# Kernel optimization log

Measured on AMD Instinct MI355X. Metric: run time of the kernel, lower is better.

Reference implementation:

```python
import jax, jax.numpy as jnp
import numpy as np

EMBED_DIM = 1024
NUM_HEADS = 16
HEAD_DIM = EMBED_DIM // NUM_HEADS  # 64, used only for score scaling
B, S = 4, 2048


def setup_inputs() -> dict:
    key = jax.random.key(0)
    k1, k2, k3, k4 = jax.random.split(key, 4)
    rotation_params = jax.random.normal(k1, (3 * EMBED_DIM * EMBED_DIM,), dtype=jnp.float32) * 0.02
    entangle_params = jax.random.normal(k2, (EMBED_DIM * EMBED_DIM,), dtype=jnp.float32) * 0.02
    inputs = jax.random.normal(k3, (B, S, EMBED_DIM), dtype=jnp.float32)
    gate_w = jax.random.normal(k4, (EMBED_DIM, EMBED_DIM), dtype=jnp.float32) * 0.02
    return {"rotation_params": rotation_params, "entangle_params": entangle_params,
            "inputs": inputs, "gate_w": gate_w}


def reference(rotation_params, entangle_params, inputs, gate_w):
    E = EMBED_DIM
    w_qkv = rotation_params.reshape(3 * E, E)   # nn.Linear weight layout (out, in)
    w_out = entangle_params.reshape(E, E)
    # qkv projection: x @ W^T, then chunk into q, k, v along last dim
    qkv = jnp.einsum('bse,fe->bsf', inputs, w_qkv)  # (B, S, 3E)
    q, k, v = jnp.split(qkv, 3, axis=-1)
    # NOTE: original code does NOT split into heads; attention over full E,
    # scaled by sqrt(head_dim).
    q = q * (1.0 / np.sqrt(HEAD_DIM)).astype(np.float32)
    scores = jnp.einsum('bqe,bke->bqk', q, k)       # (B, S, S)
    attn = jax.nn.softmax(scores, axis=-1)
    attn_out = jnp.einsum('bqk,bke->bqe', attn, v)  # (B, S, E)
    out = jnp.einsum('bse,fe->bsf', attn_out, w_out)
    gate = jax.nn.sigmoid(jnp.einsum('bse,fe->bsf', out, gate_w))
    return gate * out
```

## Files before the change

kernel.cpp:

```cpp
#include <hip/hip_runtime.h>
#include <math.h>

#define EMB 1024
#define NB 4
#define SQ 2048
#define TOK (NB*SQ)

typedef __attribute__((ext_vector_type(8))) short bhalf8;
typedef __attribute__((ext_vector_type(4))) float f32x4;

__device__ __forceinline__ unsigned short f32_to_bf16(float f) {
    unsigned int u = __float_as_uint(f);
    u += 0x7FFFu + ((u >> 16) & 1u);
    return (unsigned short)(u >> 16);
}
__device__ __forceinline__ float bf16_to_f32(unsigned short h) {
    return __uint_as_float(((unsigned int)h) << 16);
}
__device__ __forceinline__ unsigned short f32_to_f16(float f) {
    union { _Float16 h; unsigned short u; } c; c.h = (_Float16)f; return c.u;
}
__device__ __forceinline__ float f16_to_f32(unsigned short u) {
    union { _Float16 h; unsigned short u; } c; c.u = u; return (float)c.h;
}

__global__ __launch_bounds__(256) void convert_all_kernel(
    const float* __restrict__ x,  unsigned short* __restrict__ x_bf,
    const float* __restrict__ rot, const float* __restrict__ ent,
    const float* __restrict__ gw, unsigned short* __restrict__ w_bf) {
    const int EE4 = EMB * EMB / 4;
    const float* src;
    unsigned short* dst;
    float scale = 1.0f;
    int j;
    if (blockIdx.x < TOK*EMB/4/256) {
        src = x; dst = x_bf; j = blockIdx.x * 256 + threadIdx.x;
        float4 v = ((const float4*)src)[j];
        ushort4 o = { f32_to_bf16(v.x), f32_to_bf16(v.y), f32_to_bf16(v.z), f32_to_bf16(v.w) };
        ((ushort4*)dst)[j] = o;
        return;
    }
    const int i = (blockIdx.x - TOK*EMB/4/256) * 256 + threadIdx.x;
    j = i; dst = w_bf;
    if (i < 3 * EE4) {
        src = rot;
        if (i < EE4) scale = 0.125f;
    } else if (i < 4 * EE4) { src = ent; j = i - 3 * EE4; }
    else                    { src = gw;  j = i - 4 * EE4; }
    float4 v = ((const float4*)src)[j];
    ushort4 o;
    o.x = f32_to_bf16(v.x * scale);
    o.y = f32_to_bf16(v.y * scale);
    o.z = f32_to_bf16(v.z * scale);
    o.w = f32_to_bf16(v.w * scale);
    ((ushort4*)dst)[i] = o;
}

__device__ __forceinline__ void async_load16(const unsigned short* gp, unsigned short* lp) {
    __builtin_amdgcn_global_load_lds(
        (const __attribute__((address_space(1))) unsigned int*)gp,
        (__attribute__((address_space(3))) unsigned int*)lp,
        16, 0, 0);
}


#define BAR()  __builtin_amdgcn_s_barrier()
#define LGK0() do { asm volatile("s_waitcnt lgkmcnt(0)" ::: "memory"); \
                    __builtin_amdgcn_sched_barrier(0); } while (0)
#define VMC6() asm volatile("s_waitcnt vmcnt(6)" ::: "memory")
#define VMC0() asm volatile("s_waitcnt vmcnt(0)" ::: "memory")

#define STAGE_A(buf, half, kofs) do { \
    async_load16(aG0 + (half)*aH + (kofs), &As[buf][(half)*8192 +        w*512]); \
    async_load16(aG1 + (half)*aH + (kofs), &As[buf][(half)*8192 + 4096 + w*512]); \
} while (0)
#define STAGE_B(buf, half, kofs) do { \
    async_load16(bG0 + (half)*bH + (kofs), &Bs[buf][(half)*8192 +        w*512]); \
    async_load16(bG1 + (half)*bH + (kofs), &Bs[buf][(half)*8192 + 4096 + w*512]); \
} while (0)

#define READ_A(p) do { \
    af[0][0] = *(const bhalf8*)(aRd + ((p)*2    )*1024 + kqs0); \
    af[0][1] = *(const bhalf8*)(aRd + ((p)*2    )*1024 + kqs1); \
    af[1][0] = *(const bhalf8*)(aRd + ((p)*2 + 1)*1024 + kqs0); \
    af[1][1] = *(const bhalf8*)(aRd + ((p)*2 + 1)*1024 + kqs1); \
} while (0)

#define READ_B() do { \
    _Pragma("unroll") \
    for (int ni_ = 0; ni_ < 4; ++ni_) { \
        bfv[ni_][0] = *(const bhalf8*)(bRd + ni_*1024 + kqs0); \
        bfv[ni_][1] = *(const bhalf8*)(bRd + ni_*1024 + kqs1); \
    } \
} while (0)

#define MFMA16(p) do { \
    __builtin_amdgcn_s_setprio(1); \
    _Pragma("unroll") \
    for (int h_ = 0; h_ < 2; ++h_) { \
        _Pragma("unroll") \
        for (int mi_ = 0; mi_ < 2; ++mi_) { \
            _Pragma("unroll") \
            for (int ni_ = 0; ni_ < 4; ++ni_) \
                acc[(p)*2 + mi_][ni_] = __builtin_amdgcn_mfma_f32_16x16x32_bf16( \
                    af[mi_][h_], bfv[ni_][h_], acc[(p)*2 + mi_][ni_], 0, 0, 0); \
        } \
    } \
    __builtin_amdgcn_s_setprio(0); \
} while (0)

template <int MODE>
__global__ __launch_bounds__(512, 2) void gemm_nt_8p(
    const unsigned short* __restrict__ A,
    const unsigned short* __restrict__ B,
    void* __restrict__ C,
    const unsigned short* __restrict__ Obf,
    float* __restrict__ Fout,
    int M, int N, int K, int lda, int ldb, int ldc,
    long sA, long sB, long sC)
{
    __shared__ __align__(16) unsigned short As[2][16384];
    __shared__ __align__(16) unsigned short Bs[2][16384];

    const int bz = blockIdx.z;
    const unsigned short* Ab = A + (long)bz * sA;
    const unsigned short* Bb = B + (long)bz * sB;
    const int bm = blockIdx.x * 256;
    const int bn = blockIdx.y * 256;
    const int t = threadIdx.x;
    const int w = t >> 6;
    const int l = t & 63;

    const int srow = l >> 3;
    const int scol = (((l & 7) ^ (l >> 3)) * 8);

    const int fr = l & 15;
    const int kqs0 = ((((l >> 4)    ) ^ (l & 7)) * 8);
    const int kqs1 = (((4 + (l >> 4)) ^ (l & 7)) * 8);

    const int wm = (w >> 2) * 128;
    const int wn = (w & 3) * 64;

    f32x4 acc[8][4];
    f32x4 zero = {0.f, 0.f, 0.f, 0.f};
    #pragma unroll
    for (int i = 0; i < 8; ++i)
        #pragma unroll
        for (int j = 0; j < 4; ++j) acc[i][j] = zero;

    const unsigned short* aG0 = Ab + (long)(bm + (    w)*8 + srow) * lda + scol;
    const unsigned short* aG1 = Ab + (long)(bm + (8 + w)*8 + srow) * lda + scol;
    const unsigned short* bG0 = Bb + (long)(bn + (    w)*8 + srow) * ldb + scol;
    const unsigned short* bG1 = Bb + (long)(bn + (8 + w)*8 + srow) * ldb + scol;
    const long aH = (long)128 * lda;
    const long bH = (long)128 * ldb;

    const int nkt = K >> 6;

    STAGE_A(0, 0, 0);  STAGE_A(0, 1, 0);
    STAGE_B(0, 0, 0);  STAGE_B(0, 1, 0);
    STAGE_B(1, 0, 64); STAGE_B(1, 1, 64);
    STAGE_A(1, 0, 64);
    VMC6();
    BAR();

    for (int kt = 0; kt < nkt; ++kt) {
        const int cur = kt & 1, nxt = cur ^ 1;
        const unsigned short* aRd = &As[cur][(wm + fr) * 64];
        const unsigned short* bRd = &Bs[cur][(wn + fr) * 64];
        const bool s1 = (kt + 1 < nkt);
        const bool s2 = (kt + 2 < nkt);
        const int k1 = (kt + 1) << 6;
        const int k2 = (kt + 2) << 6;

        bhalf8 bfv[4][2], af[2][2];

        READ_B();
        READ_A(0);
        if (s1) STAGE_A(nxt, 1, k1);
        BAR(); LGK0();
        MFMA16(0);
        BAR();

        READ_A(1);
        if (s2) STAGE_B(cur, 0, k2);
        BAR(); LGK0();
        MFMA16(1);
        BAR();

        READ_A(2);
        if (s2) STAGE_B(cur, 1, k2);
        BAR(); LGK0();
        MFMA16(2);
        BAR();

        READ_A(3);
        if (s2) { STAGE_A(cur, 0, k2); VMC6(); }
        else    { VMC0(); }
        BAR(); LGK0();
        MFMA16(3);
        BAR();
    }

    const int crow = (l >> 4) * 4;
    const int ccol = l & 15;
    #pragma unroll
    for (int mi = 0; mi < 8; ++mi) {
        #pragma unroll
        for (int ni = 0; ni < 4; ++ni) {
            #pragma unroll
            for (int r = 0; r < 4; ++r) {
                const int gr = bm + wm + mi*16 + crow + r;
                const int gc = bn + wn + ni*16 + ccol;
                const float v = acc[mi][ni][r];
                const long idx = (long)gr * ldc + gc;
                if (MODE == 0) {
                    ((unsigned short*)C)[(long)bz*sC + idx] = f32_to_bf16(v);
                } else if (MODE == 1) {
                    ((unsigned short*)C)[(long)bz*sC + idx] = f32_to_f16(v);
                } else {
                    const float o = bf16_to_f32(Obf[idx]);
                    const float g = 1.0f / (1.0f + __expf(-v));
                    Fout[idx] = g * o;
                }
            }
        }
    }
}

#undef BAR
#undef LGK0
#undef VMC6
#undef VMC0
#undef STAGE_A
#undef STAGE_B
#undef READ_A
#undef READ_B
#undef MFMA16

__global__ __launch_bounds__(256) void softmax_kernel(const unsigned short* __restrict__ sc,
                                                      unsigned short* __restrict__ attn) {
    const long row = blockIdx.x;
    const unsigned short* p = sc + row * SQ;
    unsigned short* q = attn + row * SQ;
    const int t = threadIdx.x;
    const int w = t >> 6, l = t & 63;
    union { bhalf8 v; unsigned short u[8]; } in;
    in.v = ((const bhalf8*)p)[t];
    float f[8];
    float m = -1e30f;
    #pragma unroll
    for (int j = 0; j < 8; ++j) { f[j] = f16_to_f32(in.u[j]); m = fmaxf(m, f[j]); }
    #pragma unroll
    for (int off = 32; off; off >>= 1) m = fmaxf(m, __shfl_xor(m, off));
    __shared__ float smax[4], ssum[4];
    if (l == 0) smax[w] = m;
    __syncthreads();
    m = fmaxf(fmaxf(smax[0], smax[1]), fmaxf(smax[2], smax[3]));
    float s = 0.f;
    #pragma unroll
    for (int j = 0; j < 8; ++j) { f[j] = __expf(f[j] - m); s += f[j]; }
    #pragma unroll
    for (int off = 32; off; off >>= 1) s += __shfl_xor(s, off);
    if (l == 0) ssum[w] = s;
    __syncthreads();
    const float inv = 1.0f / (ssum[0] + ssum[1] + ssum[2] + ssum[3]);
    union { bhalf8 v; unsigned short u[8]; } o;
    #pragma unroll
    for (int j = 0; j < 8; ++j) o.u[j] = f32_to_bf16(f[j] * inv);
    ((bhalf8*)q)[t] = o.v;
}

__global__ void transpose_v(const unsigned short* __restrict__ qkv,
                            unsigned short* __restrict__ vT) {
    __shared__ unsigned short tile[32][33];
    const int b = blockIdx.z;
    const unsigned short* v = qkv + (long)b * SQ * (3*EMB) + 2*EMB;
    const int e = blockIdx.x * 32 + threadIdx.x;
    const int s = blockIdx.y * 32 + threadIdx.y;
    tile[threadIdx.y][threadIdx.x] = v[(long)s * (3*EMB) + e];
    __syncthreads();
    const int so = blockIdx.y * 32 + threadIdx.x;
    const int eo = blockIdx.x * 32 + threadIdx.y;
    vT[(long)b * EMB * SQ + (long)eo * SQ + so] = tile[threadIdx.x][threadIdx.y];
}

extern "C" void kernel_launch(void* const* d_in, const int* in_sizes, int n_in,
                              void* d_out, int out_size, void* d_ws, size_t ws_size,
                              hipStream_t stream) {
    const float* rot = (const float*)d_in[0];
    const float* ent = (const float*)d_in[1];
    const float* x   = (const float*)d_in[2];
    const float* gw  = (const float*)d_in[3];
    float* outp = (float*)d_out;
    char* ws = (char*)d_ws;

    size_t off = 0;
    unsigned short* x_bf    = (unsigned short*)(ws + off); off += (size_t)TOK*EMB*2;
    unsigned short* wqkv_bf = (unsigned short*)(ws + off); off += (size_t)3*EMB*EMB*2;
    unsigned short* wout_bf = (unsigned short*)(ws + off); off += (size_t)EMB*EMB*2;
    unsigned short* gate_bf = (unsigned short*)(ws + off); off += (size_t)EMB*EMB*2;
    unsigned short* qkv_bf  = (unsigned short*)(ws + off); off += (size_t)TOK*3*EMB*2;
    unsigned short* vT_bf   = (unsigned short*)(ws + off); off += (size_t)NB*EMB*SQ*2;
    unsigned short* sc_f16  = (unsigned short*)(ws + off); off += (size_t)NB*SQ*SQ*2;
    unsigned short* attn_bf = qkv_bf;
    unsigned short* ao_bf   = x_bf;
    unsigned short* out_bf  = qkv_bf + (size_t)NB*SQ*SQ;

    convert_all_kernel<<<dim3(TOK*EMB/4/256 + 5*EMB*EMB/4/256), dim3(256), 0, stream>>>(
        x, x_bf, rot, ent, gw, wqkv_bf);

    gemm_nt_8p<0><<<dim3(TOK/256, 3*EMB/256, 1), dim3(512), 0, stream>>>(
        x_bf, wqkv_bf, qkv_bf, nullptr, nullptr,
        TOK, 3*EMB, EMB, EMB, EMB, 3*EMB, 0, 0, 0);

    transpose_v<<<dim3(EMB/32, SQ/32, NB), dim3(32, 32), 0, stream>>>(qkv_bf, vT_bf);

    gemm_nt_8p<1><<<dim3(SQ/256, SQ/256, NB), dim3(512), 0, stream>>>(
        qkv_bf, qkv_bf + EMB, sc_f16, nullptr, nullptr,
        SQ, SQ, EMB, 3*EMB, 3*EMB, SQ,
        (long)SQ*3*EMB, (long)SQ*3*EMB, (long)SQ*SQ);

    softmax_kernel<<<dim3(NB*SQ), dim3(256), 0, stream>>>(sc_f16, attn_bf);

    gemm_nt_8p<0><<<dim3(SQ/256, EMB/256, NB), dim3(512), 0, stream>>>(
        attn_bf, vT_bf, ao_bf, nullptr, nullptr,
        SQ, EMB, SQ, SQ, SQ, EMB,
        (long)SQ*SQ, (long)EMB*SQ, (long)SQ*EMB);

    gemm_nt_8p<0><<<dim3(TOK/256, EMB/256, 1), dim3(512), 0, stream>>>(
        ao_bf, wout_bf, out_bf, nullptr, nullptr,
        TOK, EMB, EMB, EMB, EMB, EMB, 0, 0, 0);

    gemm_nt_8p<2><<<dim3(TOK/256, EMB/256, 1), dim3(512), 0, stream>>>(
        out_bf, gate_bf, nullptr, out_bf, outp,
        TOK, EMB, EMB, EMB, EMB, EMB, 0, 0, 0);
}
```

Measured before the change: 355.0 us.

## Add 128x128 single-buffer GEMM for small-N stages and reschedule 256-tile pipeline

After: 329.6 us. 7.2% less time.

```diff
diff --git a/kernel.cpp b/kernel.cpp
--- a/kernel.cpp
+++ b/kernel.cpp
@@ -63,54 +63,8 @@
         16, 0, 0);
 }
 
-
-#define BAR()  __builtin_amdgcn_s_barrier()
-#define LGK0() do { asm volatile("s_waitcnt lgkmcnt(0)" ::: "memory"); \
-                    __builtin_amdgcn_sched_barrier(0); } while (0)
-#define VMC6() asm volatile("s_waitcnt vmcnt(6)" ::: "memory")
-#define VMC0() asm volatile("s_waitcnt vmcnt(0)" ::: "memory")
-
-#define STAGE_A(buf, half, kofs) do { \
-    async_load16(aG0 + (half)*aH + (kofs), &As[buf][(half)*8192 +        w*512]); \
-    async_load16(aG1 + (half)*aH + (kofs), &As[buf][(half)*8192 + 4096 + w*512]); \
-} while (0)
-#define STAGE_B(buf, half, kofs) do { \
-    async_load16(bG0 + (half)*bH + (kofs), &Bs[buf][(half)*8192 +        w*512]); \
-    async_load16(bG1 + (half)*bH + (kofs), &Bs[buf][(half)*8192 + 4096 + w*512]); \
-} while (0)
-
-#define READ_A(p) do { \
-    af[0][0] = *(const bhalf8*)(aRd + ((p)*2    )*1024 + kqs0); \
-    af[0][1] = *(const bhalf8*)(aRd + ((p)*2    )*1024 + kqs1); \
-    af[1][0] = *(const bhalf8*)(aRd + ((p)*2 + 1)*1024 + kqs0); \
-    af[1][1] = *(const bhalf8*)(aRd + ((p)*2 + 1)*1024 + kqs1); \
-} while (0)
-
-#define READ_B() do { \
-    _Pragma("unroll") \
-    for (int ni_ = 0; ni_ < 4; ++ni_) { \
-        bfv[ni_][0] = *(const bhalf8*)(bRd + ni_*1024 + kqs0); \
-        bfv[ni_][1] = *(const bhalf8*)(bRd + ni_*1024 + kqs1); \
-    } \
-} while (0)
-
-#define MFMA16(p) do { \
-    __builtin_amdgcn_s_setprio(1); \
-    _Pragma("unroll") \
-    for (int h_ = 0; h_ < 2; ++h_) { \
-        _Pragma("unroll") \
-        for (int mi_ = 0; mi_ < 2; ++mi_) { \
-            _Pragma("unroll") \
-            for (int ni_ = 0; ni_ < 4; ++ni_) \
-                acc[(p)*2 + mi_][ni_] = __builtin_amdgcn_mfma_f32_16x16x32_bf16( \
-                    af[mi_][h_], bfv[ni_][h_], acc[(p)*2 + mi_][ni_], 0, 0, 0); \
-        } \
-    } \
-    __builtin_amdgcn_s_setprio(0); \
-} while (0)
-
 template <int MODE>
-__global__ __launch_bounds__(512, 2) void gemm_nt_8p(
+__global__ __launch_bounds__(256) void gemm_nt_128(
     const unsigned short* __restrict__ A,
     const unsigned short* __restrict__ B,
     void* __restrict__ C,
@@ -119,93 +73,68 @@
     int M, int N, int K, int lda, int ldb, int ldc,
     long sA, long sB, long sC)
 {
-    __shared__ __align__(16) unsigned short As[2][16384];
-    __shared__ __align__(16) unsigned short Bs[2][16384];
+    __shared__ __align__(16) unsigned short As[128*64];
+    __shared__ __align__(16) unsigned short Bs[128*64];
 
     const int bz = blockIdx.z;
     const unsigned short* Ab = A + (long)bz * sA;
     const unsigned short* Bb = B + (long)bz * sB;
-    const int bm = blockIdx.x * 256;
-    const int bn = blockIdx.y * 256;
+    const int bm = blockIdx.x * 128;
+    const int bn = blockIdx.y * 128;
     const int t = threadIdx.x;
     const int w = t >> 6;
     const int l = t & 63;
-
-    const int srow = l >> 3;
-    const int scol = (((l & 7) ^ (l >> 3)) * 8);
-
+    const int srow8 = l >> 3;
+    const int scol  = (((l & 7) ^ ((l >> 3) & 7)) * 8);
+
+    f32x4 zero = {0.f, 0.f, 0.f, 0.f};
+    f32x4 acc[4][4];
+    #pragma unroll
+    for (int i = 0; i < 4; ++i)
+        #pragma unroll
+        for (int j = 0; j < 4; ++j) acc[i][j] = zero;
+
+    const int wm = (w >> 1) * 64;
+    const int wn = (w & 1) * 64;
     const int fr = l & 15;
     const int kqs0 = ((((l >> 4)    ) ^ (l & 7)) * 8);
     const int kqs1 = (((4 + (l >> 4)) ^ (l & 7)) * 8);
 
-    const int wm = (w >> 2) * 128;
-    const int wn = (w & 3) * 64;
-
-    f32x4 acc[8][4];
-    f32x4 zero = {0.f, 0.f, 0.f, 0.f};
-    #pragma unroll
-    for (int i = 0; i < 8; ++i)
-        #pragma unroll
-        for (int j = 0; j < 4; ++j) acc[i][j] = zero;
-
-    const unsigned short* aG0 = Ab + (long)(bm + (    w)*8 + srow) * lda + scol;
-    const unsigned short* aG1 = Ab + (long)(bm + (8 + w)*8 + srow) * lda + scol;
-    const unsigned short* bG0 = Bb + (long)(bn + (    w)*8 + srow) * ldb + scol;
-    const unsigned short* bG1 = Bb + (long)(bn + (8 + w)*8 + srow) * ldb + scol;
-    const long aH = (long)128 * lda;
-    const long bH = (long)128 * ldb;
-
     const int nkt = K >> 6;
-
-    STAGE_A(0, 0, 0);  STAGE_A(0, 1, 0);
-    STAGE_B(0, 0, 0);  STAGE_B(0, 1, 0);
-    STAGE_B(1, 0, 64); STAGE_B(1, 1, 64);
-    STAGE_A(1, 0, 64);
-    VMC6();
-    BAR();
-
     for (int kt = 0; kt < nkt; ++kt) {
-        const int cur = kt & 1, nxt = cur ^ 1;
-        const unsigned short* aRd = &As[cur][(wm + fr) * 64];
-        const unsigned short* bRd = &Bs[cur][(wn + fr) * 64];
-        const bool s1 = (kt + 1 < nkt);
-        const bool s2 = (kt + 2 < nkt);
-        const int k1 = (kt + 1) << 6;
-        const int k2 = (kt + 2) << 6;
-
-        bhalf8 bfv[4][2], af[2][2];
-
-        READ_B();
-        READ_A(0);
-        if (s1) STAGE_A(nxt, 1, k1);
-        BAR(); LGK0();
-        MFMA16(0);
-        BAR();
-
-        READ_A(1);
-        if (s2) STAGE_B(cur, 0, k2);
-        BAR(); LGK0();
-        MFMA16(1);
-        BAR();
-
-        READ_A(2);
-        if (s2) STAGE_B(cur, 1, k2);
-        BAR(); LGK0();
-        MFMA16(2);
-        BAR();
-
-        READ_A(3);
-        if (s2) { STAGE_A(cur, 0, k2); VMC6(); }
-        else    { VMC0(); }
-        BAR(); LGK0();
-        MFMA16(3);
-        BAR();
+        const int k0 = kt << 6;
+        __syncthreads();
+        #pragma unroll
+        for (int r = 0; r < 4; ++r) {
+            const int rr = (r*4 + w) * 8 + srow8;
+            async_load16(Ab + (long)(bm + rr) * lda + (k0 + scol), As + (r*4 + w) * 512);
+            async_load16(Bb + (long)(bn + rr) * ldb + (k0 + scol), Bs + (r*4 + w) * 512);
+        }
+        __syncthreads();
+
+        #pragma unroll
+        for (int h = 0; h < 2; ++h) {
+            const int kq = h ? kqs1 : kqs0;
+            bhalf8 af[4], bfr[4];
+            #pragma unroll
+            for (int mi = 0; mi < 4; ++mi)
+                af[mi] = *(const bhalf8*)(As + (wm + mi*16 + fr) * 64 + kq);
+            #pragma unroll
+            for (int ni = 0; ni < 4; ++ni)
+                bfr[ni] = *(const bhalf8*)(Bs + (wn + ni*16 + fr) * 64 + kq);
+            #pragma unroll
+            for (int mi = 0; mi < 4; ++mi)
+                #pragma unroll
+                for (int ni = 0; ni < 4; ++ni)
+                    acc[mi][ni] = __builtin_amdgcn_mfma_f32_16x16x32_bf16(
+                        af[mi], bfr[ni], acc[mi][ni], 0, 0, 0);
+        }
     }
 
     const int crow = (l >> 4) * 4;
     const int ccol = l & 15;
     #pragma unroll
-    for (int mi = 0; mi < 8; ++mi) {
+    for (int mi = 0; mi < 4; ++mi) {
         #pragma unroll
         for (int ni = 0; ni < 4; ++ni) {
             #pragma unroll
@@ -228,8 +157,165 @@
     }
 }
 
-#undef BAR
-#undef LGK0
+
+#define BARF() asm volatile("s_barrier" ::: "memory")
+#define VMC6() asm volatile("s_waitcnt vmcnt(6)" ::: "memory")
+#define VMC0() asm volatile("s_waitcnt vmcnt(0)" ::: "memory")
+
+#define STAGE_A(buf, half, kofs) do { \
+    async_load16(aG0 + (half)*aH + (kofs), &As[buf][(half)*8192 +        w*512]); \
+    async_load16(aG1 + (half)*aH + (kofs), &As[buf][(half)*8192 + 4096 + w*512]); \
+} while (0)
+#define STAGE_B(buf, half, kofs) do { \
+    async_load16(bG0 + (half)*bH + (kofs), &Bs[buf][(half)*8192 +        w*512]); \
+    async_load16(bG1 + (half)*bH + (kofs), &Bs[buf][(half)*8192 + 4096 + w*512]); \
+} while (0)
+
+#define READ_A(p) do { \
+    af[0][0] = *(const bhalf8*)(aRd + ((p)*2    )*1024 + kqs0); \
+    af[0][1] = *(const bhalf8*)(aRd + ((p)*2    )*1024 + kqs1); \
+    af[1][0] = *(const bhalf8*)(aRd + ((p)*2 + 1)*1024 + kqs0); \
+    af[1][1] = *(const bhalf8*)(aRd + ((p)*2 + 1)*1024 + kqs1); \
+} while (0)
+
+#define READ_B() do { \
+    _Pragma("unroll") \
+    for (int ni_ = 0; ni_ < 4; ++ni_) { \
+        bfv[ni_][0] = *(const bhalf8*)(bRd + ni_*1024 + kqs0); \
+        bfv[ni_][1] = *(const bhalf8*)(bRd + ni_*1024 + kqs1); \
+    } \
+} while (0)
+
+#define MFMA16(p) do { \
+    __builtin_amdgcn_s_setprio(1); \
+    _Pragma("unroll") \
+    for (int h_ = 0; h_ < 2; ++h_) { \
+        _Pragma("unroll") \
+        for (int mi_ = 0; mi_ < 2; ++mi_) { \
+            _Pragma("unroll") \
+            for (int ni_ = 0; ni_ < 4; ++ni_) \
+                acc[(p)*2 + mi_][ni_] = __builtin_amdgcn_mfma_f32_16x16x32_bf16( \
+                    af[mi_][h_], bfv[ni_][h_], acc[(p)*2 + mi_][ni_], 0, 0, 0); \
+        } \
+    } \
+    __builtin_amdgcn_s_setprio(0); \
+} while (0)
+
+template <int MODE>
+__global__ __launch_bounds__(512, 2) void gemm_nt_8p(
+    const unsigned short* __restrict__ A,
+    const unsigned short* __restrict__ B,
+    void* __restrict__ C,
+    const unsigned short* __restrict__ Obf,
+    float* __restrict__ Fout,
+    int M, int N, int K, int lda, int ldb, int ldc,
+    long sA, long sB, long sC)
+{
+    __shared__ __align__(16) unsigned short As[2][16384];
+    __shared__ __align__(16) unsigned short Bs[2][16384];
+
+    const int bz = blockIdx.z;
+    const unsigned short* Ab = A + (long)bz * sA;
+    const unsigned short* Bb = B + (long)bz * sB;
+    const int bm = blockIdx.x * 256;
+    const int bn = blockIdx.y * 256;
+    const int t = threadIdx.x;
+    const int w = t >> 6;
+    const int l = t & 63;
+
+    const int srow = l >> 3;
+    const int scol = (((l & 7) ^ (l >> 3)) * 8);
+
+    const int fr = l & 15;
+    const int kqs0 = ((((l >> 4)    ) ^ (l & 7)) * 8);
+    const int kqs1 = (((4 + (l >> 4)) ^ (l & 7)) * 8);
+
+    const int wm = (w >> 2) * 128;
+    const int wn = (w & 3) * 64;
+
+    f32x4 acc[8][4];
+    f32x4 zero = {0.f, 0.f, 0.f, 0.f};
+    #pragma unroll
+    for (int i = 0; i < 8; ++i)
+        #pragma unroll
+        for (int j = 0; j < 4; ++j) acc[i][j] = zero;
+
+    const unsigned short* aG0 = Ab + (long)(bm + (    w)*8 + srow) * lda + scol;
+    const unsigned short* aG1 = Ab + (long)(bm + (8 + w)*8 + srow) * lda + scol;
+    const unsigned short* bG0 = Bb + (long)(bn + (    w)*8 + srow) * ldb + scol;
+    const unsigned short* bG1 = Bb + (long)(bn + (8 + w)*8 + srow) * ldb + scol;
+    const long aH = (long)128 * lda;
+    const long bH = (long)128 * ldb;
+
+    const int nkt = K >> 6;
+
+    STAGE_A(0, 0, 0);  STAGE_A(0, 1, 0);
+    STAGE_B(0, 0, 0);  STAGE_B(0, 1, 0);
+    STAGE_B(1, 0, 64); STAGE_B(1, 1, 64);
+    STAGE_A(1, 0, 64);
+    VMC6();
+    BARF();
+
+    for (int kt = 0; kt < nkt; ++kt) {
+        const int cur = kt & 1, nxt = cur ^ 1;
+        const unsigned short* aRd = &As[cur][(wm + fr) * 64];
+        const unsigned short* bRd = &Bs[cur][(wn + fr) * 64];
+        const bool s1 = (kt + 1 < nkt);
+        const bool s2 = (kt + 2 < nkt);
+        const int k1 = (kt + 1) << 6;
+        const int k2 = (kt + 2) << 6;
+
+        bhalf8 bfv[4][2], af[2][2];
+
+        if (s1) STAGE_A(nxt, 1, k1);
+        READ_B();
+        READ_A(0);
+        MFMA16(0);
+        BARF();
+
+        if (s2) STAGE_B(cur, 0, k2);
+        READ_A(1);
+        MFMA16(1);
+
+        if (s2) STAGE_B(cur, 1, k2);
+        READ_A(2);
+        MFMA16(2);
+        BARF();
+
+        if (s2) STAGE_A(cur, 0, k2);
+        READ_A(3);
+        MFMA16(3);
+        if (s2) VMC6(); else VMC0();
+        BARF();
+    }
+
+    const int crow = (l >> 4) * 4;
+    const int ccol = l & 15;
+    #pragma unroll
+    for (int mi = 0; mi < 8; ++mi) {
+        #pragma unroll
+        for (int ni = 0; ni < 4; ++ni) {
+            #pragma unroll
+            for (int r = 0; r < 4; ++r) {
+                const int gr = bm + wm + mi*16 + crow + r;
+                const int gc = bn + wn + ni*16 + ccol;
+                const float v = acc[mi][ni][r];
+                const long idx = (long)gr * ldc + gc;
+                if (MODE == 0) {
+                    ((unsigned short*)C)[(long)bz*sC + idx] = f32_to_bf16(v);
+                } else if (MODE == 1) {
+                    ((unsigned short*)C)[(long)bz*sC + idx] = f32_to_f16(v);
+                } else {
+                    const float o = bf16_to_f32(Obf[idx]);
+                    const float g = 1.0f / (1.0f + __expf(-v));
+                    Fout[idx] = g * o;
+                }
+            }
+        }
+    }
+}
+
+#undef BARF
 #undef VMC6
 #undef VMC0
 #undef STAGE_A
@@ -323,16 +409,16 @@
 
     softmax_kernel<<<dim3(NB*SQ), dim3(256), 0, stream>>>(sc_f16, attn_bf);
 
-    gemm_nt_8p<0><<<dim3(SQ/256, EMB/256, NB), dim3(512), 0, stream>>>(
+    gemm_nt_128<0><<<dim3(SQ/128, EMB/128, NB), dim3(256), 0, stream>>>(
         attn_bf, vT_bf, ao_bf, nullptr, nullptr,
         SQ, EMB, SQ, SQ, SQ, EMB,
         (long)SQ*SQ, (long)EMB*SQ, (long)SQ*EMB);
 
-    gemm_nt_8p<0><<<dim3(TOK/256, EMB/256, 1), dim3(512), 0, stream>>>(
+    gemm_nt_128<0><<<dim3(TOK/128, EMB/128, 1), dim3(256), 0, stream>>>(
         ao_bf, wout_bf, out_bf, nullptr, nullptr,
         TOK, EMB, EMB, EMB, EMB, EMB, 0, 0, 0);
 
-    gemm_nt_8p<2><<<dim3(TOK/256, EMB/256, 1), dim3(512), 0, stream>>>(
+    gemm_nt_128<2><<<dim3(TOK/128, EMB/128, 1), dim3(256), 0, stream>>>(
         out_bf, gate_bf, nullptr, out_bf, outp,
         TOK, EMB, EMB, EMB, EMB, EMB, 0, 0, 0);
 }
```
